# Kernel optimization log

Measured on AMD Instinct MI355X. Metric: run time of the kernel, lower is better.

## Reference

```python
import jax, jax.numpy as jnp
import numpy as np

DIM = 768
NUM_HEADS = 12
HEAD_DIM = DIM // NUM_HEADS
SCALE = HEAD_DIM ** -0.5


def setup_inputs() -> dict:
    key = jax.random.key(0)
    k1, k2, k3, k4, k5 = jax.random.split(key, 5)
    B, N = 1, 4096
    x = jax.random.normal(k1, (B, N, DIM), dtype=jnp.float32)
    xpos = jax.random.randint(k2, (B, N, 2), 0, 64, dtype=jnp.int64)
    # learned parameters (torch nn.Linear convention: W is [out, in])
    W_qkv = jax.random.normal(k3, (3 * DIM, DIM), dtype=jnp.float32) * 0.02
    W_proj = jax.random.normal(k4, (DIM, DIM), dtype=jnp.float32) * 0.02
    b_proj = jax.random.normal(k5, (DIM,), dtype=jnp.float32) * 0.02
    return {"x": x, "xpos": xpos, "W_qkv": W_qkv, "W_proj": W_proj, "b_proj": b_proj}


def reference(x, xpos, W_qkv, W_proj, b_proj):
    B, N, C = x.shape
    H, D = NUM_HEADS, HEAD_DIM
    # qkv projection (no bias), then split into q,k,v of shape [B,H,N,D]
    qkv = jnp.einsum('bnc,fc->bnf', x, W_qkv)            # [B,N,3C]
    qkv = qkv.reshape(B, N, 3, H, D).transpose(2, 0, 3, 1, 4)  # [3,B,H,N,D]
    q, k, v = qkv[0], qkv[1], qkv[2]
    # rope is None in this config -> q,k unchanged; xpos unused
    attn = jnp.einsum('bhnd,bhmd->bhnm', q, k) * SCALE   # [B,H,N,N]
    attn = jax.nn.softmax(attn, axis=-1)
    out = jnp.einsum('bhnm,bhmd->bhnd', attn, v)          # [B,H,N,D]
    out = out.transpose(0, 2, 1, 3).reshape(B, N, C)      # [B,N,C]
    out = jnp.einsum('bnc,oc->bno', out, W_proj) + b_proj
    return out
```

## Files before the change

### kernel.cpp

```cpp
#include <hip/hip_runtime.h>

#define DEVI __device__ __forceinline__

typedef unsigned short u16;
typedef unsigned int u32;
using u16x8 = __attribute__((ext_vector_type(8))) u16;
using u16x4 = __attribute__((ext_vector_type(4))) u16;
using u32x4 = __attribute__((ext_vector_type(4))) u32;
using bf16x8 = __attribute__((ext_vector_type(8))) __bf16;
using f32x2 = __attribute__((ext_vector_type(2))) float;
using f32x4 = __attribute__((ext_vector_type(4))) float;
using f32x16 = __attribute__((ext_vector_type(16))) float;

typedef const __attribute__((address_space(1))) u32 gu32;
typedef __attribute__((address_space(3))) u32 lu32;

#if __has_builtin(__builtin_amdgcn_exp2f)
#define EXP2(x) __builtin_amdgcn_exp2f(x)
#else
#define EXP2(x) __builtin_exp2f(x)
#endif

DEVI u16 f2bf(float f) {
    u32 u = __builtin_bit_cast(u32, f);
    u32 r = (u + 0x7fffu + ((u >> 16) & 1u)) >> 16;
    return (u16)r;
}
DEVI float bf2f(u16 b) {
    u32 u = ((u32)b) << 16;
    return __builtin_bit_cast(float, u);
}
DEVI u32 cvtpk_bf16(float lo, float hi) {
    u32 r;
    asm("v_cvt_pk_bf16_f32 %0, %1, %2" : "=v"(r) : "v"(lo), "v"(hi));
    return r;
}
DEVI f32x2 pkadd(f32x2 a, f32x2 b) {
    f32x2 d;
    asm("v_pk_add_f32 %0, %1, %2" : "=v"(d) : "v"(a), "v"(b));
    return d;
}

DEVI bf16x8 frag_ld(const u16* p) {
    return __builtin_bit_cast(bf16x8, *(const u16x8*)p);
}

DEVI void async16(const void* g, void* lds) {
    __builtin_amdgcn_global_load_lds((gu32*)g, (lu32*)lds, 16, 0, 0);
}

#define MFMA32(a, b, c) __builtin_amdgcn_mfma_f32_32x32x16_bf16(a, b, c, 0, 0, 0)

#define QK_SCALE 0.18033688011112042f

__global__ void cvt3_kernel(const float* __restrict__ s0, const float* __restrict__ s1,
                            const float* __restrict__ s2,
                            u16* __restrict__ d0, u16* __restrict__ d1, u16* __restrict__ d2,
                            int n0, int n1) {
    int i = (blockIdx.x * blockDim.x + threadIdx.x) * 4;
    const float* s; u16* d;
    if (i < n0) { s = s0; d = d0; }
    else if (i < n0 + n1) { s = s1 - n0; d = d1 - n0; }
    else { s = s2 - (n0 + n1); d = d2 - (n0 + n1); }
    float4 v = *(const float4*)(s + i);
    u16x4 o;
    o[0] = f2bf(v.x); o[1] = f2bf(v.y); o[2] = f2bf(v.z); o[3] = f2bf(v.w);
    *(u16x4*)(d + i) = o;
}

template<int MODE, int NBN, int MPX>
__global__ __launch_bounds__(256) void gemm_bt(const u16* __restrict__ A,
                                               const u16* __restrict__ B,
                                               void* __restrict__ Out,
                                               const float* __restrict__ bias,
                                               u16* __restrict__ kt,
                                               u16* __restrict__ vt2,
                                               int M, int Nn, int K) {
    const int id = blockIdx.x;
    const int xcd = id & 7, local = id >> 3;
    const int m0 = (xcd * MPX + local / NBN) * 128;
    const int n0 = (local % NBN) * 128;
    const int tid = threadIdx.x, w = tid >> 6, lane = tid & 63;
    const int l15 = lane & 15, l4 = lane >> 4;
    __shared__ __align__(16) u16 As[128 * 32];
    __shared__ __align__(16) u16 Bs[128 * 32];
    const int wm = (w >> 1) * 64, wn = (w & 1) * 64;
    f32x4 acc[4][4] = {};
    const int srow = lane >> 2;
    const int sk = (lane & 3) * 8;

    for (int kk = 0; kk < K; kk += 32) {
#pragma unroll
        for (int it = 0; it < 2; ++it) {
            const int rbase = (w * 2 + it) * 16;
            async16(A + (size_t)(m0 + rbase + srow) * K + kk + sk, &As[rbase * 32]);
            async16(B + (size_t)(n0 + rbase + srow) * K + kk + sk, &Bs[rbase * 32]);
        }
        __syncthreads();
        bf16x8 af[4], bfr[4];
#pragma unroll
        for (int i = 0; i < 4; ++i) {
            af[i] = frag_ld(&As[(wm + i * 16 + l15) * 32 + l4 * 8]);
            bfr[i] = frag_ld(&Bs[(wn + i * 16 + l15) * 32 + l4 * 8]);
        }
#pragma unroll
        for (int i = 0; i < 4; ++i)
#pragma unroll
            for (int j = 0; j < 4; ++j)
                acc[i][j] = __builtin_amdgcn_mfma_f32_16x16x32_bf16(af[i], bfr[j], acc[i][j], 0, 0, 0);
        __syncthreads();
    }
#pragma unroll
    for (int i = 0; i < 4; ++i)
#pragma unroll
        for (int j = 0; j < 4; ++j)
#pragma unroll
            for (int r = 0; r < 4; ++r) {
                const int row = m0 + wm + i * 16 + l4 * 4 + r;
                const int col = n0 + wn + j * 16 + l15;
                if (MODE == 0) {
                    const float v = acc[i][j][r];
                    if (col < 768) {
                        ((u16*)Out)[(size_t)row * Nn + col] = f2bf(v * QK_SCALE);
                    } else if (col < 1536) {
                        const int c2 = col - 768;
                        const int hh = c2 >> 6, d = c2 & 63;
                        const int s = row >> 5, l31r = row & 31;
                        const int mm = d >> 4, hb = (d >> 3) & 1, jj = d & 7;
                        kt[(((size_t)(hh * 128 + s) * 4 + mm) << 9) +
                           (hb * 32 + l31r) * 8 + jj] = f2bf(v);
                    } else {
                        const int c2 = col - 1536;
                        const int hh = c2 >> 6, d = c2 & 63;
                        const int s = row >> 5, kv = row & 31;
                        const int ks = kv >> 4, rem = kv & 15;
                        const int hv = (rem >> 2) & 1;
                        const int jv = (rem & 3) | (((rem >> 3) & 1) << 2);
                        const int Oh = d >> 5, l31v = d & 31;
                        vt2[(((size_t)(hh * 128 + s) * 4 + ks * 2 + Oh) << 9) +
                            (hv * 32 + l31v) * 8 + jv] = f2bf(v);
                    }
                } else {
                    ((float*)Out)[(size_t)row * Nn + col] = acc[i][j][r] + bias[col];
                }
            }
}

__global__ __launch_bounds__(128, 2) void attn_kernel(const u16* __restrict__ qkv,
                                                      const u16* __restrict__ kt,
                                                      const u16* __restrict__ vt2,
                                                      u16* __restrict__ op,
                                                      float* __restrict__ lsums) {
    const int id = blockIdx.x;
    const int xcd = id & 7, slot = id >> 3;
    const int gi = slot >> 5, qbi = slot & 31;
    const int g = gi * 8 + xcd;
    const int h = g % 12, sp = g / 12;
    const int tid = threadIdx.x, w = tid >> 6, lane = tid & 63;
    const int l31 = lane & 31, hi = lane >> 5;
    const int q0 = qbi * 128 + w * 64;

    bf16x8 qA0, qA1, qA2, qA3, qB0, qB1, qB2, qB3;
    {
        const u16* qp = qkv + (size_t)(q0 + l31) * 2304 + h * 64 + hi * 8;
        qA0 = frag_ld(qp); qA1 = frag_ld(qp + 16);
        qA2 = frag_ld(qp + 32); qA3 = frag_ld(qp + 48);
        const u16* qp2 = qp + (size_t)32 * 2304;
        qB0 = frag_ld(qp2); qB1 = frag_ld(qp2 + 16);
        qB2 = frag_ld(qp2 + 32); qB3 = frag_ld(qp2 + 48);
    }

    const u16* kc = kt + (size_t)(h * 128 + sp * 32) * 2048 + lane * 8;
    const u16* vc = vt2 + (size_t)(h * 128 + sp * 32) * 2048 + lane * 8;

    f32x16 O0 = {}, O1 = {}, O2 = {}, O3 = {};
    float lsumA = 0.f, lsumB = 0.f;

    bf16x8 kf0 = frag_ld(kc), kf1 = frag_ld(kc + 512),
           kf2 = frag_ld(kc + 1024), kf3 = frag_ld(kc + 1536);
    bf16x8 vf0 = frag_ld(vc), vf1 = frag_ld(vc + 512),
           vf2 = frag_ld(vc + 1024), vf3 = frag_ld(vc + 1536);
    kc += 2048; vc += 2048;

#define LSUM_TREE(E, dst)                                                       \
    {                                                                           \
        f32x2 t0_ = pkadd(__builtin_shufflevector(E, E, 0, 1),                  \
                          __builtin_shufflevector(E, E, 2, 3));                 \
        f32x2 t1_ = pkadd(__builtin_shufflevector(E, E, 4, 5),                  \
                          __builtin_shufflevector(E, E, 6, 7));                 \
        f32x2 t2_ = pkadd(__builtin_shufflevector(E, E, 8, 9),                  \
                          __builtin_shufflevector(E, E, 10, 11));               \
        f32x2 t3_ = pkadd(__builtin_shufflevector(E, E, 12, 13),                \
                          __builtin_shufflevector(E, E, 14, 15));               \
        f32x2 u0_ = pkadd(t0_, t1_);                                            \
        f32x2 u1_ = pkadd(t2_, t3_);                                            \
        f32x2 v0_ = pkadd(u0_, u1_);                                            \
        dst += v0_[0] + v0_[1];                                                 \
    }

#pragma unroll 1
    for (int s = 0; s < 32; ++s) {
        f32x16 S0 = {}, S1 = {};
        __builtin_amdgcn_s_setprio(1);
        S0 = MFMA32(kf0, qA0, S0);  S1 = MFMA32(kf0, qB0, S1);
        S0 = MFMA32(kf1, qA1, S0);  S1 = MFMA32(kf1, qB1, S1);
        S0 = MFMA32(kf2, qA2, S0);  S1 = MFMA32(kf2, qB2, S1);
        S0 = MFMA32(kf3, qA3, S0);  S1 = MFMA32(kf3, qB3, S1);
        __builtin_amdgcn_s_setprio(0);
        kf0 = frag_ld(kc); kf1 = frag_ld(kc + 512);
        kf2 = frag_ld(kc + 1024); kf3 = frag_ld(kc + 1536);
        kc += 2048;

        f32x16 E0, E1;
#pragma unroll
        for (int r = 0; r < 16; ++r) E0[r] = EXP2(S0[r]);
#pragma unroll
        for (int r = 0; r < 16; ++r) E1[r] = EXP2(S1[r]);
        u32x4 wa0 = { cvtpk_bf16(E0[0], E0[1]), cvtpk_bf16(E0[2], E0[3]),
                      cvtpk_bf16(E0[4], E0[5]), cvtpk_bf16(E0[6], E0[7]) };
        u32x4 wa1 = { cvtpk_bf16(E0[8], E0[9]), cvtpk_bf16(E0[10], E0[11]),
                      cvtpk_bf16(E0[12], E0[13]), cvtpk_bf16(E0[14], E0[15]) };
        u32x4 wb0 = { cvtpk_bf16(E1[0], E1[1]), cvtpk_bf16(E1[2], E1[3]),
                      cvtpk_bf16(E1[4], E1[5]), cvtpk_bf16(E1[6], E1[7]) };
        u32x4 wb1 = { cvtpk_bf16(E1[8], E1[9]), cvtpk_bf16(E1[10], E1[11]),
                      cvtpk_bf16(E1[12], E1[13]), cvtpk_bf16(E1[14], E1[15]) };
        bf16x8 pasA0 = __builtin_bit_cast(bf16x8, wa0);
        bf16x8 pasA1 = __builtin_bit_cast(bf16x8, wa1);
        bf16x8 pasB0 = __builtin_bit_cast(bf16x8, wb0);
        bf16x8 pasB1 = __builtin_bit_cast(bf16x8, wb1);
        LSUM_TREE(E0, lsumA)
        LSUM_TREE(E1, lsumB)

        __builtin_amdgcn_s_setprio(1);
        O0 = MFMA32(pasA0, vf0, O0);  O2 = MFMA32(pasB0, vf0, O2);
        O1 = MFMA32(pasA0, vf1, O1);  O3 = MFMA32(pasB0, vf1, O3);
        O0 = MFMA32(pasA1, vf2, O0);  O2 = MFMA32(pasB1, vf2, O2);
        O1 = MFMA32(pasA1, vf3, O1);  O3 = MFMA32(pasB1, vf3, O3);
        __builtin_amdgcn_s_setprio(0);
        vf0 = frag_ld(vc); vf1 = frag_ld(vc + 512);
        vf2 = frag_ld(vc + 1024); vf3 = frag_ld(vc + 1536);
        vc += 2048;
    }
#undef LSUM_TREE

    lsumA += __shfl_xor(lsumA, 32);
    lsumB += __shfl_xor(lsumB, 32);
    u16* ob = op + (size_t)sp * 3145728;
    const int rr4 = 4 * hi;
#pragma unroll
    for (int r = 0; r < 16; ++r) {
        const int q = (r & 3) + 8 * (r >> 2) + rr4;
        const size_t rowoff = (size_t)(q0 + q) * 768 + h * 64 + l31;
        ob[rowoff] = f2bf(O0[r]);
        ob[rowoff + 32] = f2bf(O1[r]);
        const size_t rowoff2 = rowoff + (size_t)32 * 768;
        ob[rowoff2] = f2bf(O2[r]);
        ob[rowoff2 + 32] = f2bf(O3[r]);
    }
    if (hi == 0) {
        lsums[(size_t)sp * 49152 + (size_t)(q0 + l31) * 12 + h] = lsumA;
        lsums[(size_t)sp * 49152 + (size_t)(q0 + 32 + l31) * 12 + h] = lsumB;
    }
}

__global__ __launch_bounds__(256) void combine_kernel(const u16* __restrict__ op,
                                                      const float* __restrict__ lsums,
                                                      u16* __restrict__ outb) {
    const int gid = blockIdx.x * 256 + threadIdx.x;
    const int e = gid * 8;
    const int q = e / 768, c = e % 768, h = c >> 6;
    float lt = 0.f;
#pragma unroll
    for (int sp = 0; sp < 4; ++sp) lt += lsums[(size_t)sp * 49152 + q * 12 + h];
    const float inv = 1.0f / lt;
    float acc[8] = {};
#pragma unroll
    for (int sp = 0; sp < 4; ++sp) {
        u16x8 o = *(const u16x8*)(op + (size_t)sp * 3145728 + (size_t)q * 768 + c);
#pragma unroll
        for (int jj = 0; jj < 8; ++jj) acc[jj] += bf2f(o[jj]);
    }
    u16x8 o;
#pragma unroll
    for (int jj = 0; jj < 8; ++jj) o[jj] = f2bf(acc[jj] * inv);
    *(u16x8*)(outb + e) = o;
}

extern "C" void kernel_launch(void* const* d_in, const int* in_sizes, int n_in,
                              void* d_out, int out_size, void* d_ws, size_t ws_size,
                              hipStream_t stream) {
    const float* x = (const float*)d_in[0];
    const float* Wqkv = (const float*)d_in[2];
    const float* Wproj = (const float*)d_in[3];
    const float* bproj = (const float*)d_in[4];

    u16* ws = (u16*)d_ws;
    u16* x_bf = ws;
    u16* wqkv_bf = x_bf + 3145728;
    u16* wproj_bf = wqkv_bf + 1769472;
    u16* qkv = wproj_bf + 589824;
    u16* attn_bf = qkv + 9437184;
    u16* vt2 = attn_bf + 3145728;
    u16* o_part = vt2 + 3145728;
    float* lsums = (float*)(o_part + 12582912);
    u16* kt = attn_bf;

    cvt3_kernel<<<5376, 256, 0, stream>>>(x, Wqkv, Wproj, x_bf, wqkv_bf, wproj_bf,
                                          3145728, 1769472);

    gemm_bt<0, 18, 4><<<576, 256, 0, stream>>>(x_bf, wqkv_bf, qkv, nullptr,
                                               kt, vt2, 4096, 2304, 768);
    attn_kernel<<<1536, 128, 0, stream>>>(qkv, kt, vt2, o_part, lsums);
    combine_kernel<<<1536, 256, 0, stream>>>(o_part, lsums, attn_bf);
    gemm_bt<1, 6, 4><<<192, 256, 0, stream>>>(attn_bf, wproj_bf, d_out, bproj,
                                              nullptr, nullptr, 4096, 768, 768);
}
```

Baseline: 126.9 us.

## Share double-buffered K/V tiles in LDS across four waves per attention block

The attention block grows from 2 to 4 waves, covering 256 query rows, and the grid is halved to match. Each K/V tile is now fetched once per block with async global-to-LDS copies into a double buffer, and every wave reads its fragments from LDS. Before, each wave loaded K/V fragments straight from global memory. This is meant to cut redundant global/L2 traffic for K/V, at the cost of a block-wide barrier every iteration and 16 KB of LDS per block, which may reduce overlap between waves.

```diff
diff --git a/kernel.cpp b/kernel.cpp
--- a/kernel.cpp
+++ b/kernel.cpp
@@ -146,19 +146,22 @@
             }
 }
 
-__global__ __launch_bounds__(128, 2) void attn_kernel(const u16* __restrict__ qkv,
+__global__ __launch_bounds__(256, 2) void attn_kernel(const u16* __restrict__ qkv,
                                                       const u16* __restrict__ kt,
                                                       const u16* __restrict__ vt2,
                                                       u16* __restrict__ op,
                                                       float* __restrict__ lsums) {
     const int id = blockIdx.x;
     const int xcd = id & 7, slot = id >> 3;
-    const int gi = slot >> 5, qbi = slot & 31;
+    const int gi = slot >> 4, qbi = slot & 15;
     const int g = gi * 8 + xcd;
     const int h = g % 12, sp = g / 12;
     const int tid = threadIdx.x, w = tid >> 6, lane = tid & 63;
     const int l31 = lane & 31, hi = lane >> 5;
-    const int q0 = qbi * 128 + w * 64;
+    const int q0 = qbi * 256 + w * 64;
+
+    __shared__ __align__(16) u16 Ks[2][2048];
+    __shared__ __align__(16) u16 Vs[2][2048];
 
     bf16x8 qA0, qA1, qA2, qA3, qB0, qB1, qB2, qB3;
     {
@@ -170,17 +173,14 @@
         qB2 = frag_ld(qp2 + 32); qB3 = frag_ld(qp2 + 48);
     }
 
-    const u16* kc = kt + (size_t)(h * 128 + sp * 32) * 2048 + lane * 8;
-    const u16* vc = vt2 + (size_t)(h * 128 + sp * 32) * 2048 + lane * 8;
+    const u16* ksrc = kt + (size_t)(h * 128 + sp * 32) * 2048 + w * 512 + lane * 8;
+    const u16* vsrc = vt2 + (size_t)(h * 128 + sp * 32) * 2048 + w * 512 + lane * 8;
 
     f32x16 O0 = {}, O1 = {}, O2 = {}, O3 = {};
     float lsumA = 0.f, lsumB = 0.f;
 
-    bf16x8 kf0 = frag_ld(kc), kf1 = frag_ld(kc + 512),
-           kf2 = frag_ld(kc + 1024), kf3 = frag_ld(kc + 1536);
-    bf16x8 vf0 = frag_ld(vc), vf1 = frag_ld(vc + 512),
-           vf2 = frag_ld(vc + 1024), vf3 = frag_ld(vc + 1536);
-    kc += 2048; vc += 2048;
+    async16(ksrc, &Ks[0][w * 512]);
+    async16(vsrc, &Vs[0][w * 512]);
 
 #define LSUM_TREE(E, dst)                                                       \
     {                                                                           \
@@ -200,6 +200,19 @@
 
 #pragma unroll 1
     for (int s = 0; s < 32; ++s) {
+        const int cur = s & 1;
+        __syncthreads();
+        if (s < 31) {
+            async16(ksrc + (s + 1) * 2048, &Ks[cur ^ 1][w * 512]);
+            async16(vsrc + (s + 1) * 2048, &Vs[cur ^ 1][w * 512]);
+        }
+        const u16* Kb = Ks[cur];
+        const u16* Vb = Vs[cur];
+
+        bf16x8 kf0 = frag_ld(&Kb[lane * 8]);
+        bf16x8 kf1 = frag_ld(&Kb[512 + lane * 8]);
+        bf16x8 kf2 = frag_ld(&Kb[1024 + lane * 8]);
+        bf16x8 kf3 = frag_ld(&Kb[1536 + lane * 8]);
         f32x16 S0 = {}, S1 = {};
         __builtin_amdgcn_s_setprio(1);
         S0 = MFMA32(kf0, qA0, S0);  S1 = MFMA32(kf0, qB0, S1);
@@ -207,9 +220,6 @@
         S0 = MFMA32(kf2, qA2, S0);  S1 = MFMA32(kf2, qB2, S1);
         S0 = MFMA32(kf3, qA3, S0);  S1 = MFMA32(kf3, qB3, S1);
         __builtin_amdgcn_s_setprio(0);
-        kf0 = frag_ld(kc); kf1 = frag_ld(kc + 512);
-        kf2 = frag_ld(kc + 1024); kf3 = frag_ld(kc + 1536);
-        kc += 2048;
 
         f32x16 E0, E1;
 #pragma unroll
@@ -231,15 +241,16 @@
         LSUM_TREE(E0, lsumA)
         LSUM_TREE(E1, lsumB)
 
+        bf16x8 vf0 = frag_ld(&Vb[lane * 8]);
+        bf16x8 vf1 = frag_ld(&Vb[512 + lane * 8]);
+        bf16x8 vf2 = frag_ld(&Vb[1024 + lane * 8]);
+        bf16x8 vf3 = frag_ld(&Vb[1536 + lane * 8]);
         __builtin_amdgcn_s_setprio(1);
         O0 = MFMA32(pasA0, vf0, O0);  O2 = MFMA32(pasB0, vf0, O2);
         O1 = MFMA32(pasA0, vf1, O1);  O3 = MFMA32(pasB0, vf1, O3);
         O0 = MFMA32(pasA1, vf2, O0);  O2 = MFMA32(pasB1, vf2, O2);
         O1 = MFMA32(pasA1, vf3, O1);  O3 = MFMA32(pasB1, vf3, O3);
         __builtin_amdgcn_s_setprio(0);
-        vf0 = frag_ld(vc); vf1 = frag_ld(vc + 512);
-        vf2 = frag_ld(vc + 1024); vf3 = frag_ld(vc + 1536);
-        vc += 2048;
     }
 #undef LSUM_TREE
 
@@ -310,7 +321,7 @@
 
     gemm_bt<0, 18, 4><<<576, 256, 0, stream>>>(x_bf, wqkv_bf, qkv, nullptr,
                                                kt, vt2, 4096, 2304, 768);
-    attn_kernel<<<1536, 128, 0, stream>>>(qkv, kt, vt2, o_part, lsums);
+    attn_kernel<<<768, 256, 0, stream>>>(qkv, kt, vt2, o_part, lsums);
     combine_kernel<<<1536, 256, 0, stream>>>(o_part, lsums, attn_bf);
     gemm_bt<1, 6, 4><<<192, 256, 0, stream>>>(attn_bf, wproj_bf, d_out, bproj,
                                               nullptr, nullptr, 4096, 768, 768);
```

New measurement: 124.9 us. No clear change (-1.6%).
